# Optimization experiments

Measured on AMD Instinct MI355X. Metric: run time of the kernel, lower is better.

Reference implementation:

```python
import jax, jax.numpy as jnp
import numpy as np

EPS = 1e-06

def _feature_map(x):
    # elu(x) + 1 -> strictly positive feature map
    return jax.nn.elu(x) + 1.0

def setup_inputs() -> dict:
    key = jax.random.key(0)
    kq, kk, kv = jax.random.split(key, 3)
    B, H, N, D = 1, 16, 2048, 64
    Q = jax.random.normal(kq, (B, H, N, D), dtype=jnp.float32)
    K = jax.random.normal(kk, (B, H, N, D), dtype=jnp.float32)
    V = jax.random.normal(kv, (B, H, N, D), dtype=jnp.float32)
    return {"Q": Q, "K": K, "V": V, "causal": 1}

def reference(Q, K, V, causal):
    Qf = _feature_map(Q)  # (B,H,N,D)
    Kf = _feature_map(K)  # (B,H,N,D)
    if causal:
        # prefix sums of per-position outer products K_m V_m^T  -> (B,H,N,D,Dv)
        KV_prefix = jnp.cumsum(Kf[..., :, None] * V[..., None, :], axis=2)
        Kf_prefix = jnp.cumsum(Kf, axis=2)  # (B,H,N,D)
        num = jnp.einsum('bhnd,bhnde->bhne', Qf, KV_prefix)
        den = jnp.einsum('bhnd,bhnd->bhn', Qf, Kf_prefix)[..., None]
        return num / (den + EPS)
    else:
        KV = jnp.einsum('bhnd,bhne->bhde', Kf, V)            # (B,H,D,Dv)
        num = jnp.einsum('bhnd,bhde->bhne', Qf, KV)          # (B,H,N,Dv)
        den = jnp.einsum('bhnd,bhd->bhn', Qf, Kf.sum(axis=2))[..., None]
        return num / (den + EPS)
```

## Files before the change

kernel.cpp:

```cpp
#include <hip/hip_runtime.h>

#define Hh   16
#define Nn   2048
#define Dd   64
#define DVv  64
#define Ll   64
#define Cc   (Nn / Ll)
#define HCc  (Hh * Cc)
#define EPSf 1e-6f
#define LDP  72

typedef __attribute__((ext_vector_type(8))) __bf16 bf16x8;
typedef __attribute__((ext_vector_type(4))) float  f32x4;

__device__ __forceinline__ float fmap(float x) {
    return x > 0.0f ? (x + 1.0f) : __expf(x);
}
__device__ __forceinline__ __bf16 tobf(float x) { return (__bf16)x; }

__global__ __launch_bounds__(256) void k_chunk_sums(
    const float* __restrict__ Kg, const float* __restrict__ Vg,
    float* __restrict__ Sws, float* __restrict__ zws)
{
    __shared__ __align__(16) __bf16 sKT[Dd][LDP];
    __shared__ __align__(16) __bf16 sVT[80][LDP];
    const int t  = threadIdx.x;
    const int hc = blockIdx.x;
    const float4* K4 = (const float4*)(Kg + (size_t)hc * (Ll * Dd));
    const float4* V4 = (const float4*)(Vg + (size_t)hc * (Ll * DVv));
    for (int i = t; i < (Ll * Dd) / 4; i += 256) {
        float4 k4 = K4[i];
        float4 v4 = V4[i];
        const int m  = i >> 4;
        const int c0 = (i & 15) * 4;
        sKT[c0 + 0][m] = tobf(fmap(k4.x));
        sKT[c0 + 1][m] = tobf(fmap(k4.y));
        sKT[c0 + 2][m] = tobf(fmap(k4.z));
        sKT[c0 + 3][m] = tobf(fmap(k4.w));
        sVT[c0 + 0][m] = tobf(v4.x);
        sVT[c0 + 1][m] = tobf(v4.y);
        sVT[c0 + 2][m] = tobf(v4.z);
        sVT[c0 + 3][m] = tobf(v4.w);
    }
    for (int i = t; i < 16 * LDP; i += 256) {
        const int r = i / LDP, c = i % LDP;
        sVT[64 + r][c] = (r == 0) ? (__bf16)1.0f : (__bf16)0.0f;
    }
    __syncthreads();

    const int lane = t & 63, wv = t >> 6;
    const int col = lane & 15, quad = lane >> 4;
    float* So = Sws + (size_t)hc * (Dd * DVv);
    for (int et = 0; et < 5; ++et) {
        f32x4 acc = {0.f, 0.f, 0.f, 0.f};
#pragma unroll
        for (int ks = 0; ks < 2; ++ks) {
            bf16x8 a = *(const bf16x8*)&sKT[wv * 16 + col][ks * 32 + quad * 8];
            bf16x8 b = *(const bf16x8*)&sVT[et * 16 + col][ks * 32 + quad * 8];
            acc = __builtin_amdgcn_mfma_f32_16x16x32_bf16(a, b, acc, 0, 0, 0);
        }
        if (et < 4) {
#pragma unroll
            for (int j = 0; j < 4; ++j) {
                const int d = wv * 16 + quad * 4 + j;
                So[d * DVv + et * 16 + col] = acc[j];
            }
        } else if (col == 0) {
#pragma unroll
            for (int j = 0; j < 4; ++j) {
                const int d = wv * 16 + quad * 4 + j;
                zws[hc * Dd + d] = acc[j];
            }
        }
    }
}

__global__ __launch_bounds__(256) void k_prefix(
    float* __restrict__ Sws, float* __restrict__ zws)
{
    const int idx = blockIdx.x * 256 + threadIdx.x;
    const int h  = idx >> 12;
    const int el = idx & 4095;
    float* base = Sws + ((size_t)h * Cc) * (Dd * DVv) + el;
    float v[Cc];
#pragma unroll
    for (int c = 0; c < Cc; ++c) v[c] = base[c * (Dd * DVv)];
    float run = 0.0f;
#pragma unroll
    for (int c = 0; c < Cc; ++c) { base[c * (Dd * DVv)] = run; run += v[c]; }
    if (idx < Hh * Dd) {
        const int zh = idx >> 6, zd = idx & 63;
        float* zb = zws + zh * Cc * Dd + zd;
        float zv[Cc];
#pragma unroll
        for (int c = 0; c < Cc; ++c) zv[c] = zb[c * Dd];
        float zr = 0.0f;
#pragma unroll
        for (int c = 0; c < Cc; ++c) { zb[c * Dd] = zr; zr += zv[c]; }
    }
}

__global__ __launch_bounds__(256) void k_output(
    const float* __restrict__ Qg, const float* __restrict__ Kg,
    const float* __restrict__ Vg, const float* __restrict__ Spre,
    const float* __restrict__ zpre, float* __restrict__ Og)
{
    __shared__ __align__(16) __bf16 aQ[Ll][LDP];
    __shared__ __align__(16) __bf16 aK[Ll][LDP];
    __shared__ __align__(16) __bf16 aW[Ll][LDP];
    __shared__ __align__(16) __bf16 bV[80][LDP];
    __shared__ __align__(16) __bf16 bS[80][LDP];
    const int t  = threadIdx.x;
    const int hc = blockIdx.x;
    const float4* Q4 = (const float4*)(Qg + (size_t)hc * (Ll * Dd));
    const float4* K4 = (const float4*)(Kg + (size_t)hc * (Ll * Dd));
    const float4* V4 = (const float4*)(Vg + (size_t)hc * (Ll * DVv));
    const float4* S4 = (const float4*)(Spre + (size_t)hc * (Dd * DVv));
    const float*  zp = zpre + hc * Dd;

    for (int i = t; i < (Ll * Dd) / 4; i += 256) {
        float4 q4 = Q4[i];
        float4 k4 = K4[i];
        float4 v4 = V4[i];
        float4 s4 = S4[i];
        const int m  = i >> 4;
        const int c0 = (i & 15) * 4;
        aQ[m][c0 + 0] = tobf(fmap(q4.x));
        aQ[m][c0 + 1] = tobf(fmap(q4.y));
        aQ[m][c0 + 2] = tobf(fmap(q4.z));
        aQ[m][c0 + 3] = tobf(fmap(q4.w));
        aK[m][c0 + 0] = tobf(fmap(k4.x));
        aK[m][c0 + 1] = tobf(fmap(k4.y));
        aK[m][c0 + 2] = tobf(fmap(k4.z));
        aK[m][c0 + 3] = tobf(fmap(k4.w));
        bV[c0 + 0][m] = tobf(v4.x);
        bV[c0 + 1][m] = tobf(v4.y);
        bV[c0 + 2][m] = tobf(v4.z);
        bV[c0 + 3][m] = tobf(v4.w);
        bS[c0 + 0][m] = tobf(s4.x);
        bS[c0 + 1][m] = tobf(s4.y);
        bS[c0 + 2][m] = tobf(s4.z);
        bS[c0 + 3][m] = tobf(s4.w);
    }
    for (int i = t; i < 16 * LDP; i += 256) {
        const int r = i / LDP, c = i % LDP;
        bV[64 + r][c] = (r == 0) ? (__bf16)1.0f : (__bf16)0.0f;
        bS[64 + r][c] = (r == 0 && c < Dd) ? tobf(zp[c]) : (__bf16)0.0f;
    }
    __syncthreads();

    const int lane = t & 63, wv = t >> 6;
    const int col = lane & 15, quad = lane >> 4;

#pragma unroll 1
    for (int mt = 0; mt < 4; ++mt) {
        f32x4 wacc = {0.f, 0.f, 0.f, 0.f};
#pragma unroll
        for (int ks = 0; ks < 2; ++ks) {
            bf16x8 a = *(const bf16x8*)&aQ[wv * 16 + col][ks * 32 + quad * 8];
            bf16x8 b = *(const bf16x8*)&aK[mt * 16 + col][ks * 32 + quad * 8];
            wacc = __builtin_amdgcn_mfma_f32_16x16x32_bf16(a, b, wacc, 0, 0, 0);
        }
#pragma unroll
        for (int j = 0; j < 4; ++j) {
            const int n = wv * 16 + quad * 4 + j;
            const int m = mt * 16 + col;
            aW[n][m] = tobf(m <= n ? wacc[j] : 0.0f);
        }
    }
    __syncthreads();

    f32x4 accs[5];
#pragma unroll 1
    for (int et = 0; et < 5; ++et) {
        f32x4 acc = {0.f, 0.f, 0.f, 0.f};
#pragma unroll
        for (int ks = 0; ks < 2; ++ks) {
            bf16x8 a = *(const bf16x8*)&aW[wv * 16 + col][ks * 32 + quad * 8];
            bf16x8 b = *(const bf16x8*)&bV[et * 16 + col][ks * 32 + quad * 8];
            acc = __builtin_amdgcn_mfma_f32_16x16x32_bf16(a, b, acc, 0, 0, 0);
        }
#pragma unroll
        for (int ks = 0; ks < 2; ++ks) {
            bf16x8 a = *(const bf16x8*)&aQ[wv * 16 + col][ks * 32 + quad * 8];
            bf16x8 b = *(const bf16x8*)&bS[et * 16 + col][ks * 32 + quad * 8];
            acc = __builtin_amdgcn_mfma_f32_16x16x32_bf16(a, b, acc, 0, 0, 0);
        }
        accs[et] = acc;
    }
    float dn[4];
#pragma unroll
    for (int j = 0; j < 4; ++j) dn[j] = __shfl(accs[4][j], lane & 48);

    float* Oc = Og + (size_t)hc * (Ll * DVv);
#pragma unroll
    for (int et = 0; et < 4; ++et) {
#pragma unroll
        for (int j = 0; j < 4; ++j) {
            const int n = wv * 16 + quad * 4 + j;
            Oc[n * DVv + et * 16 + col] = accs[et][j] / (dn[j] + EPSf);
        }
    }
}

extern "C" void kernel_launch(void* const* d_in, const int* in_sizes, int n_in,
                              void* d_out, int out_size, void* d_ws, size_t ws_size,
                              hipStream_t stream) {
    const float* Q = (const float*)d_in[0];
    const float* K = (const float*)d_in[1];
    const float* V = (const float*)d_in[2];
    float* Sws = (float*)d_ws;
    float* zws = Sws + (size_t)HCc * Dd * DVv;
    float* out = (float*)d_out;

    k_chunk_sums<<<HCc, 256, 0, stream>>>(K, V, Sws, zws);
    k_prefix<<<(Hh * Dd * DVv) / 256, 256, 0, stream>>>(Sws, zws);
    k_output<<<HCc, 256, 0, stream>>>(Q, K, V, Sws, zws, out);
}
```

Baseline: 89.50 us.

## Fuse chunk-sum, prefix and output kernels into one cooperative kernel

Merges the three launches into a single cooperative kernel that uses grid-wide syncs between the chunk-state, prefix-scan and output phases. Q, K and V are loaded once and kept in shared memory across phases, and one shared buffer serves as both the transposed K and the causal weight matrix. This removes two kernel launches and the repeated global reads of K and V. In exchange it pays for two grid barriers and depends on all 512 blocks being co-resident.

```diff
diff --git a/kernel.cpp b/kernel.cpp
--- a/kernel.cpp
+++ b/kernel.cpp
@@ -1,4 +1,7 @@
 #include <hip/hip_runtime.h>
+#include <hip/hip_cooperative_groups.h>
+
+namespace cg = cooperative_groups;
 
 #define Hh   16
 #define Nn   2048
@@ -11,6 +14,7 @@
 #define LDP  72
 
 typedef __attribute__((ext_vector_type(8))) __bf16 bf16x8;
+typedef __attribute__((ext_vector_type(4))) __bf16 bf16x4;
 typedef __attribute__((ext_vector_type(4))) float  f32x4;
 
 __device__ __forceinline__ float fmap(float x) {
@@ -18,139 +22,124 @@
 }
 __device__ __forceinline__ __bf16 tobf(float x) { return (__bf16)x; }
 
-__global__ __launch_bounds__(256) void k_chunk_sums(
-    const float* __restrict__ Kg, const float* __restrict__ Vg,
-    float* __restrict__ Sws, float* __restrict__ zws)
-{
-    __shared__ __align__(16) __bf16 sKT[Dd][LDP];
-    __shared__ __align__(16) __bf16 sVT[80][LDP];
-    const int t  = threadIdx.x;
-    const int hc = blockIdx.x;
-    const float4* K4 = (const float4*)(Kg + (size_t)hc * (Ll * Dd));
-    const float4* V4 = (const float4*)(Vg + (size_t)hc * (Ll * DVv));
-    for (int i = t; i < (Ll * Dd) / 4; i += 256) {
-        float4 k4 = K4[i];
-        float4 v4 = V4[i];
-        const int m  = i >> 4;
-        const int c0 = (i & 15) * 4;
-        sKT[c0 + 0][m] = tobf(fmap(k4.x));
-        sKT[c0 + 1][m] = tobf(fmap(k4.y));
-        sKT[c0 + 2][m] = tobf(fmap(k4.z));
-        sKT[c0 + 3][m] = tobf(fmap(k4.w));
-        sVT[c0 + 0][m] = tobf(v4.x);
-        sVT[c0 + 1][m] = tobf(v4.y);
-        sVT[c0 + 2][m] = tobf(v4.z);
-        sVT[c0 + 3][m] = tobf(v4.w);
-    }
-    for (int i = t; i < 16 * LDP; i += 256) {
-        const int r = i / LDP, c = i % LDP;
-        sVT[64 + r][c] = (r == 0) ? (__bf16)1.0f : (__bf16)0.0f;
-    }
-    __syncthreads();
-
-    const int lane = t & 63, wv = t >> 6;
-    const int col = lane & 15, quad = lane >> 4;
-    float* So = Sws + (size_t)hc * (Dd * DVv);
-    for (int et = 0; et < 5; ++et) {
-        f32x4 acc = {0.f, 0.f, 0.f, 0.f};
-#pragma unroll
-        for (int ks = 0; ks < 2; ++ks) {
-            bf16x8 a = *(const bf16x8*)&sKT[wv * 16 + col][ks * 32 + quad * 8];
-            bf16x8 b = *(const bf16x8*)&sVT[et * 16 + col][ks * 32 + quad * 8];
-            acc = __builtin_amdgcn_mfma_f32_16x16x32_bf16(a, b, acc, 0, 0, 0);
-        }
-        if (et < 4) {
-#pragma unroll
-            for (int j = 0; j < 4; ++j) {
-                const int d = wv * 16 + quad * 4 + j;
-                So[d * DVv + et * 16 + col] = acc[j];
-            }
-        } else if (col == 0) {
-#pragma unroll
-            for (int j = 0; j < 4; ++j) {
-                const int d = wv * 16 + quad * 4 + j;
-                zws[hc * Dd + d] = acc[j];
-            }
-        }
-    }
-}
-
-__global__ __launch_bounds__(256) void k_prefix(
-    float* __restrict__ Sws, float* __restrict__ zws)
-{
-    const int idx = blockIdx.x * 256 + threadIdx.x;
-    const int h  = idx >> 12;
-    const int el = idx & 4095;
-    float* base = Sws + ((size_t)h * Cc) * (Dd * DVv) + el;
-    float v[Cc];
-#pragma unroll
-    for (int c = 0; c < Cc; ++c) v[c] = base[c * (Dd * DVv)];
-    float run = 0.0f;
-#pragma unroll
-    for (int c = 0; c < Cc; ++c) { base[c * (Dd * DVv)] = run; run += v[c]; }
-    if (idx < Hh * Dd) {
-        const int zh = idx >> 6, zd = idx & 63;
-        float* zb = zws + zh * Cc * Dd + zd;
-        float zv[Cc];
-#pragma unroll
-        for (int c = 0; c < Cc; ++c) zv[c] = zb[c * Dd];
-        float zr = 0.0f;
-#pragma unroll
-        for (int c = 0; c < Cc; ++c) { zb[c * Dd] = zr; zr += zv[c]; }
-    }
-}
-
-__global__ __launch_bounds__(256) void k_output(
+__global__ __launch_bounds__(256) void k_fused(
     const float* __restrict__ Qg, const float* __restrict__ Kg,
-    const float* __restrict__ Vg, const float* __restrict__ Spre,
-    const float* __restrict__ zpre, float* __restrict__ Og)
+    const float* __restrict__ Vg, float* __restrict__ Sws,
+    float* __restrict__ zws, float* __restrict__ Og)
 {
     __shared__ __align__(16) __bf16 aQ[Ll][LDP];
     __shared__ __align__(16) __bf16 aK[Ll][LDP];
-    __shared__ __align__(16) __bf16 aW[Ll][LDP];
+    __shared__ __align__(16) __bf16 sT[Ll][LDP];
     __shared__ __align__(16) __bf16 bV[80][LDP];
     __shared__ __align__(16) __bf16 bS[80][LDP];
+
     const int t  = threadIdx.x;
     const int hc = blockIdx.x;
-    const float4* Q4 = (const float4*)(Qg + (size_t)hc * (Ll * Dd));
-    const float4* K4 = (const float4*)(Kg + (size_t)hc * (Ll * Dd));
-    const float4* V4 = (const float4*)(Vg + (size_t)hc * (Ll * DVv));
-    const float4* S4 = (const float4*)(Spre + (size_t)hc * (Dd * DVv));
-    const float*  zp = zpre + hc * Dd;
-
-    for (int i = t; i < (Ll * Dd) / 4; i += 256) {
-        float4 q4 = Q4[i];
-        float4 k4 = K4[i];
-        float4 v4 = V4[i];
-        float4 s4 = S4[i];
-        const int m  = i >> 4;
-        const int c0 = (i & 15) * 4;
-        aQ[m][c0 + 0] = tobf(fmap(q4.x));
-        aQ[m][c0 + 1] = tobf(fmap(q4.y));
-        aQ[m][c0 + 2] = tobf(fmap(q4.z));
-        aQ[m][c0 + 3] = tobf(fmap(q4.w));
-        aK[m][c0 + 0] = tobf(fmap(k4.x));
-        aK[m][c0 + 1] = tobf(fmap(k4.y));
-        aK[m][c0 + 2] = tobf(fmap(k4.z));
-        aK[m][c0 + 3] = tobf(fmap(k4.w));
-        bV[c0 + 0][m] = tobf(v4.x);
-        bV[c0 + 1][m] = tobf(v4.y);
-        bV[c0 + 2][m] = tobf(v4.z);
-        bV[c0 + 3][m] = tobf(v4.w);
-        bS[c0 + 0][m] = tobf(s4.x);
-        bS[c0 + 1][m] = tobf(s4.y);
-        bS[c0 + 2][m] = tobf(s4.z);
-        bS[c0 + 3][m] = tobf(s4.w);
-    }
-    for (int i = t; i < 16 * LDP; i += 256) {
-        const int r = i / LDP, c = i % LDP;
-        bV[64 + r][c] = (r == 0) ? (__bf16)1.0f : (__bf16)0.0f;
-        bS[64 + r][c] = (r == 0 && c < Dd) ? tobf(zp[c]) : (__bf16)0.0f;
-    }
-    __syncthreads();
-
     const int lane = t & 63, wv = t >> 6;
     const int col = lane & 15, quad = lane >> 4;
+    cg::grid_group grid = cg::this_grid();
+
+    {
+        const float4* Q4 = (const float4*)(Qg + (size_t)hc * (Ll * Dd));
+        const float4* K4 = (const float4*)(Kg + (size_t)hc * (Ll * Dd));
+        const float4* V4 = (const float4*)(Vg + (size_t)hc * (Ll * DVv));
+        for (int i = t; i < (Ll * Dd) / 4; i += 256) {
+            float4 q4 = Q4[i];
+            float4 k4 = K4[i];
+            float4 v4 = V4[i];
+            const int m  = i >> 4;
+            const int c0 = (i & 15) * 4;
+            float kf0 = fmap(k4.x), kf1 = fmap(k4.y), kf2 = fmap(k4.z), kf3 = fmap(k4.w);
+            bf16x4 qv = { tobf(fmap(q4.x)), tobf(fmap(q4.y)), tobf(fmap(q4.z)), tobf(fmap(q4.w)) };
+            bf16x4 kv = { tobf(kf0), tobf(kf1), tobf(kf2), tobf(kf3) };
+            *(bf16x4*)&aQ[m][c0] = qv;
+            *(bf16x4*)&aK[m][c0] = kv;
+            sT[c0 + 0][m] = kv[0];
+            sT[c0 + 1][m] = kv[1];
+            sT[c0 + 2][m] = kv[2];
+            sT[c0 + 3][m] = kv[3];
+            bV[c0 + 0][m] = tobf(v4.x);
+            bV[c0 + 1][m] = tobf(v4.y);
+            bV[c0 + 2][m] = tobf(v4.z);
+            bV[c0 + 3][m] = tobf(v4.w);
+        }
+        for (int i = t; i < 16 * LDP; i += 256) {
+            const int r = i / LDP, c = i % LDP;
+            bV[64 + r][c] = (r == 0) ? (__bf16)1.0f : (__bf16)0.0f;
+        }
+    }
+    __syncthreads();
+
+    {
+        float* So = Sws + (size_t)hc * (Dd * DVv);
+        for (int et = 0; et < 5; ++et) {
+            f32x4 acc = {0.f, 0.f, 0.f, 0.f};
+#pragma unroll
+            for (int ks = 0; ks < 2; ++ks) {
+                bf16x8 a = *(const bf16x8*)&sT[wv * 16 + col][ks * 32 + quad * 8];
+                bf16x8 b = *(const bf16x8*)&bV[et * 16 + col][ks * 32 + quad * 8];
+                acc = __builtin_amdgcn_mfma_f32_16x16x32_bf16(a, b, acc, 0, 0, 0);
+            }
+            if (et < 4) {
+#pragma unroll
+                for (int j = 0; j < 4; ++j) {
+                    const int d = wv * 16 + quad * 4 + j;
+                    So[d * DVv + et * 16 + col] = acc[j];
+                }
+            } else if (col == 0) {
+#pragma unroll
+                for (int j = 0; j < 4; ++j) {
+                    const int d = wv * 16 + quad * 4 + j;
+                    zws[hc * Dd + d] = acc[j];
+                }
+            }
+        }
+    }
+    grid.sync();
+
+    {
+        const int gid = blockIdx.x * 256 + t;
+        if (gid < Hh * Dd * DVv) {
+            const int h  = gid >> 12;
+            const int el = gid & 4095;
+            float* base = Sws + ((size_t)h * Cc) * (Dd * DVv) + el;
+            float v[Cc];
+#pragma unroll
+            for (int c = 0; c < Cc; ++c) v[c] = base[c * (Dd * DVv)];
+            float run = 0.0f;
+#pragma unroll
+            for (int c = 0; c < Cc; ++c) { base[c * (Dd * DVv)] = run; run += v[c]; }
+        }
+        if (gid < Hh * Dd) {
+            const int zh = gid >> 6, zd = gid & 63;
+            float* zb = zws + zh * Cc * Dd + zd;
+            float zv[Cc];
+#pragma unroll
+            for (int c = 0; c < Cc; ++c) zv[c] = zb[c * Dd];
+            float zr = 0.0f;
+#pragma unroll
+            for (int c = 0; c < Cc; ++c) { zb[c * Dd] = zr; zr += zv[c]; }
+        }
+    }
+    grid.sync();
+
+    {
+        const float4* S4 = (const float4*)(Sws + (size_t)hc * (Dd * DVv));
+        const float*  zp = zws + hc * Dd;
+        for (int i = t; i < (Dd * DVv) / 4; i += 256) {
+            float4 s4 = S4[i];
+            const int d  = i >> 4;
+            const int e0 = (i & 15) * 4;
+            bS[e0 + 0][d] = tobf(s4.x);
+            bS[e0 + 1][d] = tobf(s4.y);
+            bS[e0 + 2][d] = tobf(s4.z);
+            bS[e0 + 3][d] = tobf(s4.w);
+        }
+        for (int i = t; i < 16 * LDP; i += 256) {
+            const int r = i / LDP, c = i % LDP;
+            bS[64 + r][c] = (r == 0 && c < Dd) ? tobf(zp[c]) : (__bf16)0.0f;
+        }
+    }
 
 #pragma unroll 1
     for (int mt = 0; mt < 4; ++mt) {
@@ -165,7 +154,7 @@
         for (int j = 0; j < 4; ++j) {
             const int n = wv * 16 + quad * 4 + j;
             const int m = mt * 16 + col;
-            aW[n][m] = tobf(m <= n ? wacc[j] : 0.0f);
+            sT[n][m] = tobf(m <= n ? wacc[j] : 0.0f);
         }
     }
     __syncthreads();
@@ -176,7 +165,7 @@
         f32x4 acc = {0.f, 0.f, 0.f, 0.f};
 #pragma unroll
         for (int ks = 0; ks < 2; ++ks) {
-            bf16x8 a = *(const bf16x8*)&aW[wv * 16 + col][ks * 32 + quad * 8];
+            bf16x8 a = *(const bf16x8*)&sT[wv * 16 + col][ks * 32 + quad * 8];
             bf16x8 b = *(const bf16x8*)&bV[et * 16 + col][ks * 32 + quad * 8];
             acc = __builtin_amdgcn_mfma_f32_16x16x32_bf16(a, b, acc, 0, 0, 0);
         }
@@ -213,7 +202,8 @@
     float* zws = Sws + (size_t)HCc * Dd * DVv;
     float* out = (float*)d_out;
 
-    k_chunk_sums<<<HCc, 256, 0, stream>>>(K, V, Sws, zws);
-    k_prefix<<<(Hh * Dd * DVv) / 256, 256, 0, stream>>>(Sws, zws);
-    k_output<<<HCc, 256, 0, stream>>>(Q, K, V, Sws, zws, out);
+    void* args[] = { (void*)&Q, (void*)&K, (void*)&V,
+                     (void*)&Sws, (void*)&zws, (void*)&out };
+    hipLaunchCooperativeKernel((const void*)k_fused, dim3(HCc), dim3(256),
+                               args, 0, stream);
 }
```

Result: slower. 225.0 us (+151.4%).

## Fuse chunk-state prefix scan into output kernel with bf16 transposed state

Applied to the files above, without the earlier changes.

Removes the separate prefix-sum kernel. Each output block now sums the per-chunk KV states of all preceding chunks directly. Chunk states are stored as transposed bf16 instead of fp32, which halves workspace traffic and lets the state tile go straight into the MFMA operand layout. Smem stores for Q and K are vectorized. The cost is redundant work: later chunks re-read up to 31 prior states, which is quadratic in chunk count and gives an imbalanced load across blocks. The bf16 partial states also add rounding error.

```diff
diff --git a/kernel.cpp b/kernel.cpp
--- a/kernel.cpp
+++ b/kernel.cpp
@@ -11,6 +11,7 @@
 #define LDP  72
 
 typedef __attribute__((ext_vector_type(8))) __bf16 bf16x8;
+typedef __attribute__((ext_vector_type(4))) __bf16 bf16x4;
 typedef __attribute__((ext_vector_type(4))) float  f32x4;
 
 __device__ __forceinline__ float fmap(float x) {
@@ -20,7 +21,7 @@
 
 __global__ __launch_bounds__(256) void k_chunk_sums(
     const float* __restrict__ Kg, const float* __restrict__ Vg,
-    float* __restrict__ Sws, float* __restrict__ zws)
+    __bf16* __restrict__ SwsT, float* __restrict__ zws)
 {
     __shared__ __align__(16) __bf16 sKT[Dd][LDP];
     __shared__ __align__(16) __bf16 sVT[80][LDP];
@@ -50,7 +51,7 @@
 
     const int lane = t & 63, wv = t >> 6;
     const int col = lane & 15, quad = lane >> 4;
-    float* So = Sws + (size_t)hc * (Dd * DVv);
+    __bf16* So = SwsT + (size_t)hc * (Dd * DVv);
     for (int et = 0; et < 5; ++et) {
         f32x4 acc = {0.f, 0.f, 0.f, 0.f};
 #pragma unroll
@@ -60,97 +61,86 @@
             acc = __builtin_amdgcn_mfma_f32_16x16x32_bf16(a, b, acc, 0, 0, 0);
         }
         if (et < 4) {
-#pragma unroll
-            for (int j = 0; j < 4; ++j) {
-                const int d = wv * 16 + quad * 4 + j;
-                So[d * DVv + et * 16 + col] = acc[j];
-            }
+            const int e = et * 16 + col;
+            const int d = wv * 16 + quad * 4;
+            bf16x4 s4 = { tobf(acc[0]), tobf(acc[1]), tobf(acc[2]), tobf(acc[3]) };
+            *(bf16x4*)&So[e * Dd + d] = s4;
         } else if (col == 0) {
 #pragma unroll
-            for (int j = 0; j < 4; ++j) {
-                const int d = wv * 16 + quad * 4 + j;
-                zws[hc * Dd + d] = acc[j];
-            }
-        }
-    }
-}
-
-__global__ __launch_bounds__(256) void k_prefix(
-    float* __restrict__ Sws, float* __restrict__ zws)
-{
-    const int idx = blockIdx.x * 256 + threadIdx.x;
-    const int h  = idx >> 12;
-    const int el = idx & 4095;
-    float* base = Sws + ((size_t)h * Cc) * (Dd * DVv) + el;
-    float v[Cc];
-#pragma unroll
-    for (int c = 0; c < Cc; ++c) v[c] = base[c * (Dd * DVv)];
-    float run = 0.0f;
-#pragma unroll
-    for (int c = 0; c < Cc; ++c) { base[c * (Dd * DVv)] = run; run += v[c]; }
-    if (idx < Hh * Dd) {
-        const int zh = idx >> 6, zd = idx & 63;
-        float* zb = zws + zh * Cc * Dd + zd;
-        float zv[Cc];
-#pragma unroll
-        for (int c = 0; c < Cc; ++c) zv[c] = zb[c * Dd];
-        float zr = 0.0f;
-#pragma unroll
-        for (int c = 0; c < Cc; ++c) { zb[c * Dd] = zr; zr += zv[c]; }
+            for (int j = 0; j < 4; ++j)
+                zws[hc * Dd + wv * 16 + quad * 4 + j] = acc[j];
+        }
     }
 }
 
 __global__ __launch_bounds__(256) void k_output(
     const float* __restrict__ Qg, const float* __restrict__ Kg,
-    const float* __restrict__ Vg, const float* __restrict__ Spre,
-    const float* __restrict__ zpre, float* __restrict__ Og)
+    const float* __restrict__ Vg, const __bf16* __restrict__ SwsT,
+    const float* __restrict__ zws, float* __restrict__ Og)
 {
     __shared__ __align__(16) __bf16 aQ[Ll][LDP];
     __shared__ __align__(16) __bf16 aK[Ll][LDP];
-    __shared__ __align__(16) __bf16 aW[Ll][LDP];
+    __shared__ __align__(16) __bf16 sW[Ll][LDP];
     __shared__ __align__(16) __bf16 bV[80][LDP];
     __shared__ __align__(16) __bf16 bS[80][LDP];
     const int t  = threadIdx.x;
     const int hc = blockIdx.x;
-    const float4* Q4 = (const float4*)(Qg + (size_t)hc * (Ll * Dd));
-    const float4* K4 = (const float4*)(Kg + (size_t)hc * (Ll * Dd));
-    const float4* V4 = (const float4*)(Vg + (size_t)hc * (Ll * DVv));
-    const float4* S4 = (const float4*)(Spre + (size_t)hc * (Dd * DVv));
-    const float*  zp = zpre + hc * Dd;
-
-    for (int i = t; i < (Ll * Dd) / 4; i += 256) {
-        float4 q4 = Q4[i];
-        float4 k4 = K4[i];
-        float4 v4 = V4[i];
-        float4 s4 = S4[i];
-        const int m  = i >> 4;
-        const int c0 = (i & 15) * 4;
-        aQ[m][c0 + 0] = tobf(fmap(q4.x));
-        aQ[m][c0 + 1] = tobf(fmap(q4.y));
-        aQ[m][c0 + 2] = tobf(fmap(q4.z));
-        aQ[m][c0 + 3] = tobf(fmap(q4.w));
-        aK[m][c0 + 0] = tobf(fmap(k4.x));
-        aK[m][c0 + 1] = tobf(fmap(k4.y));
-        aK[m][c0 + 2] = tobf(fmap(k4.z));
-        aK[m][c0 + 3] = tobf(fmap(k4.w));
-        bV[c0 + 0][m] = tobf(v4.x);
-        bV[c0 + 1][m] = tobf(v4.y);
-        bV[c0 + 2][m] = tobf(v4.z);
-        bV[c0 + 3][m] = tobf(v4.w);
-        bS[c0 + 0][m] = tobf(s4.x);
-        bS[c0 + 1][m] = tobf(s4.y);
-        bS[c0 + 2][m] = tobf(s4.z);
-        bS[c0 + 3][m] = tobf(s4.w);
-    }
-    for (int i = t; i < 16 * LDP; i += 256) {
-        const int r = i / LDP, c = i % LDP;
-        bV[64 + r][c] = (r == 0) ? (__bf16)1.0f : (__bf16)0.0f;
-        bS[64 + r][c] = (r == 0 && c < Dd) ? tobf(zp[c]) : (__bf16)0.0f;
-    }
-    __syncthreads();
-
+    const int h  = hc >> 5, c = hc & 31;
     const int lane = t & 63, wv = t >> 6;
     const int col = lane & 15, quad = lane >> 4;
+
+    {
+        const float4* Q4 = (const float4*)(Qg + (size_t)hc * (Ll * Dd));
+        const float4* K4 = (const float4*)(Kg + (size_t)hc * (Ll * Dd));
+        const float4* V4 = (const float4*)(Vg + (size_t)hc * (Ll * DVv));
+        for (int i = t; i < (Ll * Dd) / 4; i += 256) {
+            float4 q4 = Q4[i];
+            float4 k4 = K4[i];
+            float4 v4 = V4[i];
+            const int m  = i >> 4;
+            const int c0 = (i & 15) * 4;
+            bf16x4 qv = { tobf(fmap(q4.x)), tobf(fmap(q4.y)), tobf(fmap(q4.z)), tobf(fmap(q4.w)) };
+            bf16x4 kv = { tobf(fmap(k4.x)), tobf(fmap(k4.y)), tobf(fmap(k4.z)), tobf(fmap(k4.w)) };
+            *(bf16x4*)&aQ[m][c0] = qv;
+            *(bf16x4*)&aK[m][c0] = kv;
+            bV[c0 + 0][m] = tobf(v4.x);
+            bV[c0 + 1][m] = tobf(v4.y);
+            bV[c0 + 2][m] = tobf(v4.z);
+            bV[c0 + 3][m] = tobf(v4.w);
+        }
+        for (int i = t; i < 16 * LDP; i += 256) {
+            const int r = i / LDP, cc = i % LDP;
+            bV[64 + r][cc] = (r == 0) ? (__bf16)1.0f : (__bf16)0.0f;
+        }
+    }
+
+    {
+        const __bf16* Sb = SwsT + ((size_t)(h * Cc)) * (Dd * DVv) + t * 16;
+        float racc[16];
+#pragma unroll
+        for (int j = 0; j < 16; ++j) racc[j] = 0.0f;
+        for (int cc = 0; cc < c; ++cc) {
+            bf16x8 s0 = *(const bf16x8*)(Sb + (size_t)cc * (Dd * DVv));
+            bf16x8 s1 = *(const bf16x8*)(Sb + (size_t)cc * (Dd * DVv) + 8);
+#pragma unroll
+            for (int j = 0; j < 8; ++j) { racc[j] += (float)s0[j]; racc[8 + j] += (float)s1[j]; }
+        }
+        const int e = t >> 2, d0 = (t & 3) * 16;
+#pragma unroll
+        for (int j = 0; j < 16; ++j) bS[e][d0 + j] = tobf(racc[j]);
+
+        if (t < Dd) {
+            const float* zb = zws + (h * Cc) * Dd + t;
+            float zr = 0.0f;
+            for (int cc = 0; cc < c; ++cc) zr += zb[cc * Dd];
+            bS[64][t] = tobf(zr);
+        }
+        for (int i = t; i < 16 * LDP; i += 256) {
+            const int r = i / LDP, cc = i % LDP;
+            if (!(r == 0 && cc < Dd)) bS[64 + r][cc] = (__bf16)0.0f;
+        }
+    }
+    __syncthreads();
 
 #pragma unroll 1
     for (int mt = 0; mt < 4; ++mt) {
@@ -165,7 +155,7 @@
         for (int j = 0; j < 4; ++j) {
             const int n = wv * 16 + quad * 4 + j;
             const int m = mt * 16 + col;
-            aW[n][m] = tobf(m <= n ? wacc[j] : 0.0f);
+            sW[n][m] = tobf(m <= n ? wacc[j] : 0.0f);
         }
     }
     __syncthreads();
@@ -176,7 +166,7 @@
         f32x4 acc = {0.f, 0.f, 0.f, 0.f};
 #pragma unroll
         for (int ks = 0; ks < 2; ++ks) {
-            bf16x8 a = *(const bf16x8*)&aW[wv * 16 + col][ks * 32 + quad * 8];
+            bf16x8 a = *(const bf16x8*)&sW[wv * 16 + col][ks * 32 + quad * 8];
             bf16x8 b = *(const bf16x8*)&bV[et * 16 + col][ks * 32 + quad * 8];
             acc = __builtin_amdgcn_mfma_f32_16x16x32_bf16(a, b, acc, 0, 0, 0);
         }
@@ -209,11 +199,10 @@
     const float* Q = (const float*)d_in[0];
     const float* K = (const float*)d_in[1];
     const float* V = (const float*)d_in[2];
-    float* Sws = (float*)d_ws;
-    float* zws = Sws + (size_t)HCc * Dd * DVv;
+    __bf16* SwsT = (__bf16*)d_ws;
+    float*  zws  = (float*)((char*)d_ws + (size_t)HCc * Dd * DVv * sizeof(__bf16));
     float* out = (float*)d_out;
 
-    k_chunk_sums<<<HCc, 256, 0, stream>>>(K, V, Sws, zws);
-    k_prefix<<<(Hh * Dd * DVv) / 256, 256, 0, stream>>>(Sws, zws);
-    k_output<<<HCc, 256, 0, stream>>>(Q, K, V, Sws, zws, out);
-}
+    k_chunk_sums<<<HCc, 256, 0, stream>>>(K, V, SwsT, zws);
+    k_output<<<HCc, 256, 0, stream>>>(Q, K, V, SwsT, zws, out);
+}
```

New measurement: 95.07 us. +6.2%, slower.
